# Optimization experiments

Measured on AMD Instinct MI355X. Metric: run time of the kernel, lower is better.

The kernel has to match this reference:

```python
import jax, jax.numpy as jnp
import numpy as np

B, H, W, C, O = 64, 32, 32, 256, 512
K = 3          # convfilterSize
EPS = 1e-3     # keras BatchNormalization default epsilon
ALPHA = 0.2    # LeakyReLU alpha


def setup_inputs() -> dict:
    key = jax.random.key(0)
    k0, k1, k2 = jax.random.split(key, 3)
    x_real = jax.random.normal(k0, (B, H, W, C), jnp.float32)
    x_imag = jax.random.normal(k1, (B, H, W, C), jnp.float32)
    # RandomNormal(mean=0.5, stddev=2.0)
    weight_time = 0.5 + 2.0 * jax.random.normal(k2, (K, K, C, O), jnp.float32)
    ones = jnp.ones((O,), jnp.float32)
    zeros = jnp.zeros((O,), jnp.float32)
    return {
        "x_real": x_real, "x_imag": x_imag, "weight_time": weight_time,
        "gamma_r": ones, "beta_r": zeros, "mean_r": zeros, "var_r": ones,
        "gamma_i": ones, "beta_i": zeros, "mean_i": zeros, "var_i": ones,
    }


def _bn_lrelu(x, gamma, beta, mean, var):
    # BatchNormalization (inference) over last axis + LeakyReLU(0.2)
    y = (x - mean) * (gamma * jax.lax.rsqrt(var + EPS)) + beta
    return jnp.where(y >= 0, y, ALPHA * y)


def reference(x_real, x_imag, weight_time,
              gamma_r, beta_r, mean_r, var_r,
              gamma_i, beta_i, mean_i, var_i):
    Hd, Wd = x_real.shape[1], x_real.shape[2]
    k = weight_time.shape[0]
    # zero-pad 3x3 kernel to full spatial size (top-left placement)
    w_pad = jnp.pad(weight_time, ((0, Hd - k), (0, Wd - k), (0, 0), (0, 0)))
    # FFT2D over spatial dims: (H,W,C,O) -> (C,O,H,W) -> fft2 -> back
    w_freq = jnp.fft.fft2(w_pad.transpose(2, 3, 0, 1).astype(jnp.complex64), axes=(-2, -1))
    w_real = w_freq.real.transpose(2, 3, 0, 1)  # (H,W,C,O)
    w_imag = w_freq.imag.transpose(2, 3, 0, 1)  # (H,W,C,O)
    # complex 'dot': channel contraction at every spatial location
    # (original broadcasts to [H,B,W,C,O] then reduce_sums over C)
    out_r = (jnp.einsum('bhwc,hwco->bhwo', x_real, w_real)
             + jnp.einsum('bhwc,hwco->bhwo', x_imag, w_imag))
    out_i = (jnp.einsum('bhwc,hwco->bhwo', x_real, w_imag)
             - jnp.einsum('bhwc,hwco->bhwo', x_imag, w_real))
    out_r = _bn_lrelu(out_r, gamma_r, beta_r, mean_r, var_r)
    out_i = _bn_lrelu(out_i, gamma_i, beta_i, mean_i, var_i)
    return (out_r, out_i)
```

## Files before the change

### kernel.cpp

```cpp
#include <hip/hip_runtime.h>
#include <hip/hip_bf16.h>

#define HH 32
#define WW 32
#define CC 256
#define OO 512
#define BB 64
#define HWC (HH*WW*CC)
#define HWO (HH*WW*OO)
#define EPS 1e-3f
#define ALPHA 0.2f

typedef __attribute__((ext_vector_type(8))) short short8;
typedef __attribute__((ext_vector_type(4))) float f32x4;
typedef __attribute__((ext_vector_type(2))) float float2v;
typedef __attribute__((ext_vector_type(4))) unsigned uint4_;

__device__ __forceinline__ short f2bf(float f) {
    return (short)__builtin_bit_cast(unsigned short, __float2bfloat16(f));
}

__global__ __launch_bounds__(256) void transpose_taps(const float* __restrict__ w,
                                                      short* __restrict__ tt) {
    __shared__ float tile[64][65];
    const int bid = blockIdx.x;
    const int t  = bid >> 5;
    const int ct = (bid >> 3) & 3;
    const int ob = bid & 7;
    const int c0 = ct * 64, o0 = ob * 64;
    const int tid = threadIdx.x;
    const int col = tid & 63;
    const int rq  = tid >> 6;
    #pragma unroll
    for (int r = 0; r < 16; ++r) {
        int c_loc = r * 4 + rq;
        tile[c_loc][col] = w[(size_t)(t * CC + c0 + c_loc) * OO + o0 + col];
    }
    __syncthreads();
    #pragma unroll
    for (int r = 0; r < 16; ++r) {
        int o_loc = r * 4 + rq;
        tt[(size_t)(t * OO + o0 + o_loc) * CC + c0 + col] = f2bf(tile[col][o_loc]);
    }
}

__global__ __launch_bounds__(512, 4) void cdot_mfma(
    const float* __restrict__ xr, const float* __restrict__ xi,
    const short* __restrict__ taps,
    const float* __restrict__ gr, const float* __restrict__ br,
    const float* __restrict__ mr, const float* __restrict__ vr,
    const float* __restrict__ gi, const float* __restrict__ bi,
    const float* __restrict__ mi_, const float* __restrict__ vi,
    float* __restrict__ outr, float* __restrict__ outi)
{
    __shared__ short sx[8192];
    __shared__ short sw[16384];

    const int tid  = threadIdx.x;
    const int lane = tid & 63;
    const int wave = tid >> 6;
    const int laneO = lane & 15;
    const int laneW = lane >> 4;

    const int p   = blockIdx.x;
    const int xcd = p & 7;
    const int r_  = p >> 3;
    const int uv  = xcd * 128 + (r_ >> 2);
    const int ot  = r_ & 3;
    const int u = uv >> 5, v = uv & 31;
    const int o0 = ot * 128;
    const int owave = o0 + wave * 16;

    float cs[9], sn[9];
    #pragma unroll
    for (int pp = 0; pp < 3; ++pp) {
        #pragma unroll
        for (int qq = 0; qq < 3; ++qq) {
            int k = (u*pp + v*qq) & 31;
            float a = (float)k * 0.0625f;
            cs[pp*3+qq] = cospif(a);
            sn[pp*3+qq] = -sinpif(a);
        }
    }

    f32x4 accR[4], accI[4];
    #pragma unroll
    for (int m = 0; m < 4; ++m) { accR[m] = (f32x4)(0.0f); accI[m] = (f32x4)(0.0f); }

    const int c8w = (tid & 7) * 8;
    const int orw = tid >> 3;

    #pragma unroll
    for (int ch = 0; ch < 4; ++ch) {
        const int kc0 = ch * 64;
        __syncthreads();

        #pragma unroll
        for (int it = 0; it < 2; ++it) {
            int s  = tid + it * 512;
            int ri = s >> 9;
            int rr = s & 511;
            int b  = rr >> 3;
            int c8 = (rr & 7) * 8;
            const float* src = (ri ? xi : xr) + (size_t)b * HWC + uv * CC + kc0 + c8;
            float4 f0 = *(const float4*)src;
            float4 f1 = *(const float4*)(src + 4);
            short8 pk;
            pk[0]=f2bf(f0.x); pk[1]=f2bf(f0.y); pk[2]=f2bf(f0.z); pk[3]=f2bf(f0.w);
            pk[4]=f2bf(f1.x); pk[5]=f2bf(f1.y); pk[6]=f2bf(f1.z); pk[7]=f2bf(f1.w);
            int idx = ri * 4096 + b * 64 + (c8 ^ ((b & 7) * 8));
            *(short8*)(sx + idx) = pk;
        }

        #pragma unroll
        for (int pass = 0; pass < 2; ++pass) {
            const int ol = orw + pass * 64;
            const short* tb = taps + (size_t)(o0 + ol) * CC + kc0 + c8w;
            float2v ar[4], ai[4];
            #pragma unroll
            for (int j = 0; j < 4; ++j) { ar[j] = (float2v)(0.0f); ai[j] = (float2v)(0.0f); }
            #pragma unroll
            for (int t = 0; t < 9; ++t) {
                short8 tp = *(const short8*)(tb + (size_t)t * (OO * CC));
                uint4_ tu = __builtin_bit_cast(uint4_, tp);
                float2v cst = (float2v)(cs[t]);
                float2v snt = (float2v)(sn[t]);
                #pragma unroll
                for (int j = 0; j < 4; ++j) {
                    unsigned uw = tu[j];
                    float2v f;
                    f.x = __uint_as_float(uw << 16);
                    f.y = __uint_as_float(uw & 0xffff0000u);
                    ar[j] = __builtin_elementwise_fma(cst, f, ar[j]);
                    ai[j] = __builtin_elementwise_fma(snt, f, ai[j]);
                }
            }
            short8 pR, pI;
            #pragma unroll
            for (int j = 0; j < 4; ++j) {
                pR[2*j]   = f2bf(ar[j].x);
                pR[2*j+1] = f2bf(ar[j].y);
                pI[2*j]   = f2bf(ai[j].x);
                pI[2*j+1] = f2bf(ai[j].y);
            }
            int widx = ol * 64 + (c8w ^ ((ol & 7) * 8));
            *(short8*)(sw + widx)        = pR;
            *(short8*)(sw + 8192 + widx) = pI;
        }
        __syncthreads();

        #pragma unroll
        for (int ks = 0; ks < 2; ++ks) {
            const int ol  = wave * 16 + laneO;
            const int cpr = (ks * 32 + laneW * 8) ^ ((ol & 7) * 8);
            short8 bR = *(const short8*)(sw + ol * 64 + cpr);
            short8 bI = *(const short8*)(sw + 8192 + ol * 64 + cpr);
            uint4_ bu = __builtin_bit_cast(uint4_, bR);
            bu ^= 0x80008000u;
            short8 bRn = __builtin_bit_cast(short8, bu);

            const int cidx = (ks * 32 + laneW * 8) ^ ((laneO & 7) * 8);
            __builtin_amdgcn_s_setprio(1);
            #pragma unroll
            for (int m = 0; m < 4; ++m) {
                int b = m * 16 + laneO;
                short8 a0 = *(const short8*)(sx + b * 64 + cidx);
                short8 a1 = *(const short8*)(sx + 4096 + b * 64 + cidx);
                accR[m] = __builtin_amdgcn_mfma_f32_16x16x32_bf16(a0, bR,  accR[m], 0, 0, 0);
                accR[m] = __builtin_amdgcn_mfma_f32_16x16x32_bf16(a1, bI,  accR[m], 0, 0, 0);
                accI[m] = __builtin_amdgcn_mfma_f32_16x16x32_bf16(a0, bI,  accI[m], 0, 0, 0);
                accI[m] = __builtin_amdgcn_mfma_f32_16x16x32_bf16(a1, bRn, accI[m], 0, 0, 0);
            }
            __builtin_amdgcn_s_setprio(0);
        }
    }

    {
        const int o = owave + laneO;
        float scR = gr[o] * rsqrtf(vr[o] + EPS);
        float mR = mr[o], bR_ = br[o];
        float scI = gi[o] * rsqrtf(vi[o] + EPS);
        float mI = mi_[o], bI_ = bi[o];
        #pragma unroll
        for (int m = 0; m < 4; ++m) {
            #pragma unroll
            for (int e = 0; e < 4; ++e) {
                int b = m * 16 + laneW * 4 + e;
                size_t idx = (size_t)b * HWO + (size_t)uv * OO + o;
                float yr = (accR[m][e] - mR) * scR + bR_;
                outr[idx] = (yr >= 0.f) ? yr : ALPHA * yr;
                float yi = (accI[m][e] - mI) * scI + bI_;
                outi[idx] = (yi >= 0.f) ? yi : ALPHA * yi;
            }
        }
    }
}

extern "C" void kernel_launch(void* const* d_in, const int* in_sizes, int n_in,
                              void* d_out, int out_size, void* d_ws, size_t ws_size,
                              hipStream_t stream) {
    const float* xr = (const float*)d_in[0];
    const float* xi = (const float*)d_in[1];
    const float* w  = (const float*)d_in[2];
    const float* gr = (const float*)d_in[3];
    const float* br = (const float*)d_in[4];
    const float* mr = (const float*)d_in[5];
    const float* vr = (const float*)d_in[6];
    const float* gi = (const float*)d_in[7];
    const float* bi = (const float*)d_in[8];
    const float* mi_ = (const float*)d_in[9];
    const float* vi = (const float*)d_in[10];

    short* taps_t = (short*)d_ws;
    float* outr = (float*)d_out;
    float* outi = outr + (size_t)BB * HWO;

    transpose_taps<<<288, 256, 0, stream>>>(w, taps_t);
    cdot_mfma<<<4096, 512, 0, stream>>>(xr, xi, taps_t,
                                        gr, br, mr, vr,
                                        gi, bi, mi_, vi,
                                        outr, outi);
}
```

Before: 299.6 us.

## Keep transposed taps in fp32 and overlap x loads with tap combination

The transposed 3x3 taps are now stored in fp32 instead of bf16, which removes the bit-unpacking ALU work in the per-frequency weight synthesis but doubles the bytes read for taps. The x tile loads are precomputed and issued after the first weight-synthesis pass, so their global latency overlaps with the tap FMAs before conversion to bf16 into LDS. There is also a small accuracy change, since taps are combined in fp32 before rounding.

```diff
diff --git a/kernel.cpp b/kernel.cpp
--- a/kernel.cpp
+++ b/kernel.cpp
@@ -13,7 +13,6 @@
 
 typedef __attribute__((ext_vector_type(8))) short short8;
 typedef __attribute__((ext_vector_type(4))) float f32x4;
-typedef __attribute__((ext_vector_type(2))) float float2v;
 typedef __attribute__((ext_vector_type(4))) unsigned uint4_;
 
 __device__ __forceinline__ short f2bf(float f) {
@@ -21,7 +20,7 @@
 }
 
 __global__ __launch_bounds__(256) void transpose_taps(const float* __restrict__ w,
-                                                      short* __restrict__ tt) {
+                                                      float* __restrict__ tt) {
     __shared__ float tile[64][65];
     const int bid = blockIdx.x;
     const int t  = bid >> 5;
@@ -40,13 +39,13 @@
     #pragma unroll
     for (int r = 0; r < 16; ++r) {
         int o_loc = r * 4 + rq;
-        tt[(size_t)(t * OO + o0 + o_loc) * CC + c0 + col] = f2bf(tile[col][o_loc]);
+        tt[(size_t)(t * OO + o0 + o_loc) * CC + c0 + col] = tile[col][o_loc];
     }
 }
 
 __global__ __launch_bounds__(512, 4) void cdot_mfma(
     const float* __restrict__ xr, const float* __restrict__ xi,
-    const short* __restrict__ taps,
+    const float* __restrict__ taps,
     const float* __restrict__ gr, const float* __restrict__ br,
     const float* __restrict__ mr, const float* __restrict__ vr,
     const float* __restrict__ gi, const float* __restrict__ bi,
@@ -90,62 +89,75 @@
     const int c8w = (tid & 7) * 8;
     const int orw = tid >> 3;
 
+    int sb[2], sc8[2], sidx[2];
+    const float* ssrc[2];
+    #pragma unroll
+    for (int it = 0; it < 2; ++it) {
+        int s  = tid + it * 512;
+        int ri = s >> 9;
+        int rr = s & 511;
+        int b  = rr >> 3;
+        int c8 = (rr & 7) * 8;
+        sb[it] = b; sc8[it] = c8;
+        ssrc[it] = (ri ? xi : xr) + (size_t)b * HWC + uv * CC + c8;
+        sidx[it] = ri * 4096 + b * 64 + (c8 ^ ((b & 7) * 8));
+    }
+
     #pragma unroll
     for (int ch = 0; ch < 4; ++ch) {
         const int kc0 = ch * 64;
         __syncthreads();
 
-        #pragma unroll
-        for (int it = 0; it < 2; ++it) {
-            int s  = tid + it * 512;
-            int ri = s >> 9;
-            int rr = s & 511;
-            int b  = rr >> 3;
-            int c8 = (rr & 7) * 8;
-            const float* src = (ri ? xi : xr) + (size_t)b * HWC + uv * CC + kc0 + c8;
-            float4 f0 = *(const float4*)src;
-            float4 f1 = *(const float4*)(src + 4);
-            short8 pk;
-            pk[0]=f2bf(f0.x); pk[1]=f2bf(f0.y); pk[2]=f2bf(f0.z); pk[3]=f2bf(f0.w);
-            pk[4]=f2bf(f1.x); pk[5]=f2bf(f1.y); pk[6]=f2bf(f1.z); pk[7]=f2bf(f1.w);
-            int idx = ri * 4096 + b * 64 + (c8 ^ ((b & 7) * 8));
-            *(short8*)(sx + idx) = pk;
-        }
+        f32x4 xf[4];
 
         #pragma unroll
         for (int pass = 0; pass < 2; ++pass) {
             const int ol = orw + pass * 64;
-            const short* tb = taps + (size_t)(o0 + ol) * CC + kc0 + c8w;
-            float2v ar[4], ai[4];
-            #pragma unroll
-            for (int j = 0; j < 4; ++j) { ar[j] = (float2v)(0.0f); ai[j] = (float2v)(0.0f); }
+            const float* tb = taps + (size_t)(o0 + ol) * CC + kc0 + c8w;
+            f32x4 ar0 = (f32x4)(0.0f), ar1 = (f32x4)(0.0f);
+            f32x4 ai0 = (f32x4)(0.0f), ai1 = (f32x4)(0.0f);
             #pragma unroll
             for (int t = 0; t < 9; ++t) {
-                short8 tp = *(const short8*)(tb + (size_t)t * (OO * CC));
-                uint4_ tu = __builtin_bit_cast(uint4_, tp);
-                float2v cst = (float2v)(cs[t]);
-                float2v snt = (float2v)(sn[t]);
-                #pragma unroll
-                for (int j = 0; j < 4; ++j) {
-                    unsigned uw = tu[j];
-                    float2v f;
-                    f.x = __uint_as_float(uw << 16);
-                    f.y = __uint_as_float(uw & 0xffff0000u);
-                    ar[j] = __builtin_elementwise_fma(cst, f, ar[j]);
-                    ai[j] = __builtin_elementwise_fma(snt, f, ai[j]);
-                }
+                const float* tp = tb + (size_t)t * (OO * CC);
+                f32x4 f0 = *(const f32x4*)tp;
+                f32x4 f1 = *(const f32x4*)(tp + 4);
+                f32x4 cst = (f32x4)(cs[t]);
+                f32x4 snt = (f32x4)(sn[t]);
+                ar0 = __builtin_elementwise_fma(cst, f0, ar0);
+                ai0 = __builtin_elementwise_fma(snt, f0, ai0);
+                ar1 = __builtin_elementwise_fma(cst, f1, ar1);
+                ai1 = __builtin_elementwise_fma(snt, f1, ai1);
             }
             short8 pR, pI;
             #pragma unroll
             for (int j = 0; j < 4; ++j) {
-                pR[2*j]   = f2bf(ar[j].x);
-                pR[2*j+1] = f2bf(ar[j].y);
-                pI[2*j]   = f2bf(ai[j].x);
-                pI[2*j+1] = f2bf(ai[j].y);
+                pR[j]   = f2bf(ar0[j]);
+                pR[4+j] = f2bf(ar1[j]);
+                pI[j]   = f2bf(ai0[j]);
+                pI[4+j] = f2bf(ai1[j]);
             }
             int widx = ol * 64 + (c8w ^ ((ol & 7) * 8));
             *(short8*)(sw + widx)        = pR;
             *(short8*)(sw + 8192 + widx) = pI;
+
+            if (pass == 0) {
+                #pragma unroll
+                for (int it = 0; it < 2; ++it) {
+                    xf[2*it]   = *(const f32x4*)(ssrc[it] + kc0);
+                    xf[2*it+1] = *(const f32x4*)(ssrc[it] + kc0 + 4);
+                }
+            }
+        }
+
+        #pragma unroll
+        for (int it = 0; it < 2; ++it) {
+            short8 pk;
+            #pragma unroll
+            for (int j = 0; j < 4; ++j) {
+                pk[j]   = f2bf(xf[2*it][j]);
+                pk[4+j] = f2bf(xf[2*it+1][j]);
+            }
+            *(short8*)(sx + sidx[it]) = pk;
         }
         __syncthreads();
 
@@ -211,7 +223,7 @@
     const float* mi_ = (const float*)d_in[9];
     const float* vi = (const float*)d_in[10];
 
-    short* taps_t = (short*)d_ws;
+    float* taps_t = (float*)d_ws;
     float* outr = (float*)d_out;
     float* outi = outr + (size_t)BB * HWO;
 
```

New measurement: 411.5 us. 37.3% more time.

## Factor 2D DFT of taps into separable column pass precomputed per frequency

Applied to the files above, without the earlier changes.

The 3x3 tap DFT is split into two separable stages. A prep kernel now computes the column-direction partial transform for all 32 v frequencies and each row p, writing complex bf16 tables (gR, gI). The main kernel then does only a 3-term complex combine over u instead of a 9-tap sum. This cuts per-block FMA work but grows the workspace tables from 9 to 192 slices of O*C. The main kernel reads six bf16 vectors per pass instead of nine, and the prep kernel becomes much larger with more global traffic.

```diff
diff --git a/kernel.cpp b/kernel.cpp
--- a/kernel.cpp
+++ b/kernel.cpp
@@ -10,6 +10,7 @@
 #define HWO (HH*WW*OO)
 #define EPS 1e-3f
 #define ALPHA 0.2f
+#define PST (OO*CC)
 
 typedef __attribute__((ext_vector_type(8))) short short8;
 typedef __attribute__((ext_vector_type(4))) float f32x4;
@@ -20,33 +21,59 @@
     return (short)__builtin_bit_cast(unsigned short, __float2bfloat16(f));
 }
 
-__global__ __launch_bounds__(256) void transpose_taps(const float* __restrict__ w,
-                                                      short* __restrict__ tt) {
-    __shared__ float tile[64][65];
+__global__ __launch_bounds__(256) void build_g(const float* __restrict__ w,
+                                               short* __restrict__ gR,
+                                               short* __restrict__ gI) {
+    __shared__ float tile[3][64][65];
     const int bid = blockIdx.x;
-    const int t  = bid >> 5;
-    const int ct = (bid >> 3) & 3;
-    const int ob = bid & 7;
+    const int ob  = bid & 7;
+    const int ct  = (bid >> 3) & 3;
+    const int vp  = bid >> 5;
+    const int p_  = vp % 3;
+    const int v_  = vp / 3;
     const int c0 = ct * 64, o0 = ob * 64;
     const int tid = threadIdx.x;
     const int col = tid & 63;
     const int rq  = tid >> 6;
-    #pragma unroll
-    for (int r = 0; r < 16; ++r) {
-        int c_loc = r * 4 + rq;
-        tile[c_loc][col] = w[(size_t)(t * CC + c0 + c_loc) * OO + o0 + col];
-    }
+
+    float csq[3], snq[3];
+    #pragma unroll
+    for (int q = 0; q < 3; ++q) {
+        int k = (v_ * q) & 31;
+        float a = (float)k * 0.0625f;
+        csq[q] = cospif(a);
+        snq[q] = sinpif(a);
+    }
+
+    #pragma unroll
+    for (int q = 0; q < 3; ++q)
+        #pragma unroll
+        for (int r = 0; r < 16; ++r) {
+            int c_loc = r * 4 + rq;
+            tile[q][c_loc][col] =
+                w[(size_t)((p_ * 3 + q) * CC + c0 + c_loc) * OO + o0 + col];
+        }
     __syncthreads();
+
     #pragma unroll
     for (int r = 0; r < 16; ++r) {
         int o_loc = r * 4 + rq;
-        tt[(size_t)(t * OO + o0 + o_loc) * CC + c0 + col] = f2bf(tile[col][o_loc]);
+        float sR = 0.f, sI = 0.f;
+        #pragma unroll
+        for (int q = 0; q < 3; ++q) {
+            float wv = tile[q][col][o_loc];
+            sR = fmaf(wv, csq[q], sR);
+            sI = fmaf(-wv, snq[q], sI);
+        }
+        size_t oidx = ((size_t)(v_ * 3 + p_) * OO + o0 + o_loc) * CC + c0 + col;
+        gR[oidx] = f2bf(sR);
+        gI[oidx] = f2bf(sI);
     }
 }
 
 __global__ __launch_bounds__(512, 4) void cdot_mfma(
     const float* __restrict__ xr, const float* __restrict__ xi,
-    const short* __restrict__ taps,
+    const short* __restrict__ gR, const short* __restrict__ gI,
     const float* __restrict__ gr, const float* __restrict__ br,
     const float* __restrict__ mr, const float* __restrict__ vr,
     const float* __restrict__ gi, const float* __restrict__ bi,
@@ -71,17 +98,10 @@
     const int o0 = ot * 128;
     const int owave = o0 + wave * 16;
 
-    float cs[9], sn[9];
-    #pragma unroll
-    for (int pp = 0; pp < 3; ++pp) {
-        #pragma unroll
-        for (int qq = 0; qq < 3; ++qq) {
-            int k = (u*pp + v*qq) & 31;
-            float a = (float)k * 0.0625f;
-            cs[pp*3+qq] = cospif(a);
-            sn[pp*3+qq] = -sinpif(a);
-        }
-    }
+    const float cu1 = cospif((float)((u) & 31) * 0.0625f);
+    const float su1 = sinpif((float)((u) & 31) * 0.0625f);
+    const float cu2 = cospif((float)((2 * u) & 31) * 0.0625f);
+    const float su2 = sinpif((float)((2 * u) & 31) * 0.0625f);
 
     f32x4 accR[4], accI[4];
     #pragma unroll
@@ -115,33 +135,50 @@
         #pragma unroll
         for (int pass = 0; pass < 2; ++pass) {
             const int ol = orw + pass * 64;
-            const short* tb = taps + (size_t)(o0 + ol) * CC + kc0 + c8w;
-            float2v ar[4], ai[4];
-            #pragma unroll
-            for (int j = 0; j < 4; ++j) { ar[j] = (float2v)(0.0f); ai[j] = (float2v)(0.0f); }
-            #pragma unroll
-            for (int t = 0; t < 9; ++t) {
-                short8 tp = *(const short8*)(tb + (size_t)t * (OO * CC));
-                uint4_ tu = __builtin_bit_cast(uint4_, tp);
-                float2v cst = (float2v)(cs[t]);
-                float2v snt = (float2v)(sn[t]);
-                #pragma unroll
-                for (int j = 0; j < 4; ++j) {
-                    unsigned uw = tu[j];
-                    float2v f;
-                    f.x = __uint_as_float(uw << 16);
-                    f.y = __uint_as_float(uw & 0xffff0000u);
-                    ar[j] = __builtin_elementwise_fma(cst, f, ar[j]);
-                    ai[j] = __builtin_elementwise_fma(snt, f, ai[j]);
-                }
-            }
+            const size_t gb = ((size_t)(v * 3) * OO + (size_t)(o0 + ol)) * CC
+                            + kc0 + c8w;
+            short8 t0R = *(const short8*)(gR + gb);
+            short8 t0I = *(const short8*)(gI + gb);
+            short8 t1R = *(const short8*)(gR + gb + PST);
+            short8 t1I = *(const short8*)(gI + gb + PST);
+            short8 t2R = *(const short8*)(gR + gb + 2 * PST);
+            short8 t2I = *(const short8*)(gI + gb + 2 * PST);
+            uint4_ u0R = __builtin_bit_cast(uint4_, t0R);
+            uint4_ u0I = __builtin_bit_cast(uint4_, t0I);
+            uint4_ u1R = __builtin_bit_cast(uint4_, t1R);
+            uint4_ u1I = __builtin_bit_cast(uint4_, t1I);
+            uint4_ u2R = __builtin_bit_cast(uint4_, t2R);
+            uint4_ u2I = __builtin_bit_cast(uint4_, t2I);
+
+            const float2v cu1v = (float2v)(cu1), su1v = (float2v)(su1), ns1v = (float2v)(-su1);
+            const float2v cu2v = (float2v)(cu2), su2v = (float2v)(su2), ns2v = (float2v)(-su2);
+
             short8 pR, pI;
             #pragma unroll
             for (int j = 0; j < 4; ++j) {
-                pR[2*j]   = f2bf(ar[j].x);
-                pR[2*j+1] = f2bf(ar[j].y);
-                pI[2*j]   = f2bf(ai[j].x);
-                pI[2*j+1] = f2bf(ai[j].y);
+                float2v f0R, f0I, f1R, f1I, f2R, f2I;
+                unsigned a;
+                a = u0R[j]; f0R.x = __uint_as_float(a << 16); f0R.y = __uint_as_float(a & 0xffff0000u);
+                a = u0I[j]; f0I.x = __uint_as_float(a << 16); f0I.y = __uint_as_float(a & 0xffff0000u);
+                a = u1R[j]; f1R.x = __uint_as_float(a << 16); f1R.y = __uint_as_float(a & 0xffff0000u);
+                a = u1I[j]; f1I.x = __uint_as_float(a << 16); f1I.y = __uint_as_float(a & 0xffff0000u);
+                a = u2R[j]; f2R.x = __uint_as_float(a << 16); f2R.y = __uint_as_float(a & 0xffff0000u);
+                a = u2I[j]; f2I.x = __uint_as_float(a << 16); f2I.y = __uint_as_float(a & 0xffff0000u);
+
+                float2v ar = f0R, ai = f0I;
+                ar = __builtin_elementwise_fma(cu1v, f1R, ar);
+                ar = __builtin_elementwise_fma(su1v, f1I, ar);
+                ai = __builtin_elementwise_fma(cu1v, f1I, ai);
+                ai = __builtin_elementwise_fma(ns1v, f1R, ai);
+                ar = __builtin_elementwise_fma(cu2v, f2R, ar);
+                ar = __builtin_elementwise_fma(su2v, f2I, ar);
+                ai = __builtin_elementwise_fma(cu2v, f2I, ai);
+                ai = __builtin_elementwise_fma(ns2v, f2R, ai);
+
+                pR[2*j]   = f2bf(ar.x);
+                pR[2*j+1] = f2bf(ar.y);
+                pI[2*j]   = f2bf(ai.x);
+                pI[2*j+1] = f2bf(ai.y);
             }
             int widx = ol * 64 + (c8w ^ ((ol & 7) * 8));
             *(short8*)(sw + widx)        = pR;
@@ -211,12 +248,13 @@
     const float* mi_ = (const float*)d_in[9];
     const float* vi = (const float*)d_in[10];
 
-    short* taps_t = (short*)d_ws;
+    short* gRp = (short*)d_ws;
+    short* gIp = gRp + (size_t)32 * 3 * OO * CC;
     float* outr = (float*)d_out;
     float* outi = outr + (size_t)BB * HWO;
 
-    transpose_taps<<<288, 256, 0, stream>>>(w, taps_t);
-    cdot_mfma<<<4096, 512, 0, stream>>>(xr, xi, taps_t,
+    build_g<<<3072, 256, 0, stream>>>(w, gRp, gIp);
+    cdot_mfma<<<4096, 512, 0, stream>>>(xr, xi, gRp, gIp,
                                         gr, br, mr, vr,
                                         gi, bi, mi_, vi,
                                         outr, outi);
```

After: 319.6 us. +6.7%, slower.
